# Optimization experiments

Measured on AMD Instinct MI355X. Metric: run time of the kernel, lower is better.

## Reference

```python
import jax, jax.numpy as jnp
import numpy as np
import math

T, B, D, H, FF = 2048, 2, 1024, 16, 4096
HD = D // H
STD = 0.02


def _gelu(x):
    # SongNet gelu: tanh approximation
    return 0.5 * x * (1.0 + jnp.tanh(math.sqrt(2.0 / math.pi) * (x + 0.044715 * x ** 3)))


def _layer_norm(x, g, b, eps=1e-5):
    mu = jnp.mean(x, axis=-1, keepdims=True)
    var = jnp.mean((x - mu) ** 2, axis=-1, keepdims=True)
    return (x - mu) * jax.lax.rsqrt(var + eps) * g + b


def setup_inputs() -> dict:
    key = jax.random.key(0)
    ks = jax.random.split(key, 6)
    return {
        "x": jax.random.normal(ks[0], (T, B, D), jnp.float32),
        "attn_mask": jnp.triu(jnp.ones((T, T), bool), k=1),  # True = masked (causal)
        "in_proj_w": jax.random.normal(ks[1], (3 * D, D), jnp.float32) * STD,
        "in_proj_b": jnp.zeros((3 * D,), jnp.float32),
        "out_w": jax.random.normal(ks[2], (D, D), jnp.float32) * STD,
        "out_b": jnp.zeros((D,), jnp.float32),
        "fc1_w": jax.random.normal(ks[3], (FF, D), jnp.float32) * STD,
        "fc1_b": jnp.zeros((FF,), jnp.float32),
        "fc2_w": jax.random.normal(ks[4], (D, FF), jnp.float32) * STD,
        "fc2_b": jnp.zeros((D,), jnp.float32),
        "ln1_g": jnp.ones((D,), jnp.float32),
        "ln1_b": jnp.zeros((D,), jnp.float32),
        "ln2_g": jnp.ones((D,), jnp.float32),
        "ln2_b": jnp.zeros((D,), jnp.float32),
    }


def reference(x, attn_mask, in_proj_w, in_proj_b, out_w, out_b,
              fc1_w, fc1_b, fc2_w, fc2_b, ln1_g, ln1_b, ln2_g, ln2_b):
    t, b, d = x.shape
    scaling = HD ** -0.5
    # fused in-proj (qkv_same path): [T,B,3D]
    qkv = x @ in_proj_w.T + in_proj_b
    q, k, v = jnp.split(qkv, 3, axis=-1)
    q = q * scaling

    def to_heads(z):  # [T,B,D] -> [B*H, T, HD]
        return z.reshape(t, b * H, HD).transpose(1, 0, 2)

    q, k, v = to_heads(q), to_heads(k), to_heads(v)
    # [B*H, T, T] attention scores (full matrix, as in original bmm)
    scores = jnp.einsum('nth,nsh->nts', q, k)
    scores = jnp.where(attn_mask[None, :, :], -jnp.inf, scores)
    w = jax.nn.softmax(scores, axis=-1)
    attn = jnp.einsum('nts,nsh->nth', w, v)          # [B*H, T, HD]
    attn = attn.transpose(1, 0, 2).reshape(t, b, d)  # [T,B,D]
    attn = attn @ out_w.T + out_b

    h = _layer_norm(x + attn, ln1_g, ln1_b)
    ff = _gelu(h @ fc1_w.T + fc1_b) @ fc2_w.T + fc2_b
    out = _layer_norm(h + ff, ln2_g, ln2_b)
    return out
```

## Files before the change

### kernel.cpp

```cpp
#include <hip/hip_runtime.h>
#include <hip/hip_bf16.h>
#include <math.h>


typedef __bf16 bf16x8_t __attribute__((ext_vector_type(8)));
typedef __bf16 bf16x4_t __attribute__((ext_vector_type(4)));
typedef float  f32x4_t  __attribute__((ext_vector_type(4)));

#define T_  2048
#define B_  2
#define D_  1024
#define H_  16
#define HD_ 64
#define FF_ 4096
#define M_  (T_ * B_)

#define LOG2E 1.4426950408889634f
#define SCL   (0.125f * LOG2E)

__device__ __forceinline__ float gelu_f(float v) {
    const float y = 0.79788456080286535588f * (v + 0.044715f * v * v * v);
    const float t = __builtin_amdgcn_exp2f(-2.8853900817779268f * y);
    return v * __builtin_amdgcn_rcpf(1.0f + t);
}

__device__ __forceinline__ void gld_lds16(const void* g, void* l) {
    __builtin_amdgcn_global_load_lds((const __attribute__((address_space(1))) void*)g,
                                     (__attribute__((address_space(3))) void*)l, 16, 0, 0);
}

template<int MODE, int OWNM>
__global__ __launch_bounds__(256, 4)
void gemm_bt(const __bf16* __restrict__ A, const __bf16* __restrict__ W,
             const float* __restrict__ bias, float* __restrict__ Cf0,
             float* __restrict__ Cf1, __bf16* __restrict__ Cb, int M, int N, int K)
{
    __shared__ __align__(16) __bf16 As[128 * 32];
    __shared__ __align__(16) __bf16 Bs[128 * 32];
    const int tid  = threadIdx.x;
    const int lane = tid & 63;
    const int wave = tid >> 6;
    const int quad = lane >> 4;
    const int l15  = lane & 15;

    const int gx = gridDim.x, gy = gridDim.y;
    int flat = ((int)blockIdx.z * gy + (int)blockIdx.y) * gx + (int)blockIdx.x;
    int bx, by, z;
    if (OWNM) {
        const int P = gy >> 3;
        const int x = flat & 7; int s = flat >> 3;
        by = x * P + (s % P); s /= P;
        bx = s % gx; z = s / gx;
    } else {
        const int P = gx >> 3;
        const int x = flat & 7; int s = flat >> 3;
        bx = x * P + (s % P); s /= P;
        by = s % gy; z = s / gy;
    }
    const int m0 = by * 128;
    const int n0 = bx * 128;
    const int wm = (wave >> 1) * 64;
    const int wn = (wave & 1) * 64;
    const int Kloc = K / (int)gridDim.z;
    const int kbeg = z * Kloc;

    const int srow = wave * 32 + (lane >> 2);
    const int scol = (((lane & 3) ^ ((lane >> 3) & 3))) * 8;
    const __bf16* gA = A + (size_t)(m0 + srow) * K + scol;
    const __bf16* gB = W + (size_t)(n0 + srow) * K + scol;
    const size_t rowK16 = (size_t)16 * K;
    __bf16* ldsA0 = As + wave * 1024;
    __bf16* ldsA1 = As + wave * 1024 + 512;
    __bf16* ldsB0 = Bs + wave * 1024;
    __bf16* ldsB1 = Bs + wave * 1024 + 512;

    const int asw = (quad ^ ((l15 >> 1) & 3)) * 8;

    f32x4_t acc[4][4] = {};

    for (int kb = kbeg; kb < kbeg + Kloc; kb += 32) {
        gld_lds16(gA + kb,          ldsA0);
        gld_lds16(gA + kb + rowK16, ldsA1);
        gld_lds16(gB + kb,          ldsB0);
        gld_lds16(gB + kb + rowK16, ldsB1);
        __syncthreads();
        bf16x8_t af[4], bfr[4];
        #pragma unroll
        for (int i = 0; i < 4; ++i) af[i]  = *(const bf16x8_t*)&As[(wm + i * 16 + l15) * 32 + asw];
        #pragma unroll
        for (int i = 0; i < 4; ++i) bfr[i] = *(const bf16x8_t*)&Bs[(wn + i * 16 + l15) * 32 + asw];
        #pragma unroll
        for (int mi = 0; mi < 4; ++mi)
            #pragma unroll
            for (int ni = 0; ni < 4; ++ni)
                acc[mi][ni] = __builtin_amdgcn_mfma_f32_16x16x32_bf16(af[mi], bfr[ni], acc[mi][ni], 0, 0, 0);
        __syncthreads();
    }

    float* __restrict__ Cf = (z == 0) ? Cf0 : Cf1;
    #pragma unroll
    for (int mi = 0; mi < 4; ++mi) {
        const int row = m0 + wm + mi * 16 + quad * 4;
        #pragma unroll
        for (int ni = 0; ni < 4; ++ni) {
            const int col = n0 + wn + ni * 16 + l15;
            const float bv = (z == 0) ? bias[col] : 0.f;
            #pragma unroll
            for (int r = 0; r < 4; ++r) {
                float v = acc[mi][ni][r] + bv;
                if (MODE == 2) v = gelu_f(v);
                if (MODE == 0) Cf[(size_t)(row + r) * N + col] = v;
                else           Cb[(size_t)(row + r) * N + col] = (__bf16)v;
            }
        }
    }
}

__global__ __launch_bounds__(256)
void vtrans_kernel(const __bf16* __restrict__ qkv, __bf16* __restrict__ vt)
{
    __shared__ __bf16 S[64][72];
    const int tt = blockIdx.x, bh = blockIdx.y;
    const int b = bh >> 4, h = bh & 15;
    const int tid = threadIdx.x;
    const int tl = tid >> 2, ch = (tid & 3) * 16;
    const __bf16* src = qkv + ((size_t)(tt * 64 + tl) * B_ + b) * (3 * D_) + 2 * D_ + h * HD_ + ch;
    *(bf16x8_t*)&S[tl][ch]     = *(const bf16x8_t*)src;
    *(bf16x8_t*)&S[tl][ch + 8] = *(const bf16x8_t*)(src + 8);
    __syncthreads();
    #pragma unroll
    for (int p = 0; p < 2; ++p) {
        const int hd = p * 32 + (tid >> 3);
        const int tc = (tid & 7) * 8;
        bf16x8_t v;
        #pragma unroll
        for (int j = 0; j < 8; ++j) v[j] = S[tc + j][hd];
        *(bf16x8_t*)(vt + ((size_t)bh * 64 + hd) * T_ + tt * 64 + tc) = v;
    }
}

__global__ __launch_bounds__(256)
void attn_kernel(const __bf16* __restrict__ qkv, const __bf16* __restrict__ vt,
                 __bf16* __restrict__ attnout)
{
    const int bh = blockIdx.y;
    const int b  = bh >> 4;
    const int h  = bh & 15;
    const int tid  = threadIdx.x;
    const int lane = tid & 63;
    const int wave = tid >> 6;
    const int quad = lane >> 4;
    const int l15  = lane & 15;

    __shared__ __align__(16) __bf16 Ks[64 * 64];
    __shared__ __align__(16) __bf16 Vs[64 * 64];
    __shared__ __align__(16) __bf16 Ps[4][16 * 64];

    const int kr = lane >> 3;
    const int kc = (lane & 7) ^ kr;
    const size_t krow = (size_t)B_ * 3 * D_;
    const __bf16* gK0 = qkv + ((size_t)(wave * 16 + kr) * B_ + b) * (3 * D_) + D_ + h * HD_ + kc * 8;
    const __bf16* gV0 = vt + ((size_t)bh * 64 + wave * 16 + kr) * T_ + kc * 8;
    __bf16* ldsK0 = &Ks[wave * 16 * 64];
    __bf16* ldsK1 = &Ks[wave * 16 * 64 + 8 * 64];
    __bf16* ldsV0 = &Vs[wave * 16 * 64];
    __bf16* ldsV1 = &Vs[wave * 16 * 64 + 8 * 64];
    const int ksw = l15 & 7;

    const bf16x8_t ONES = {(__bf16)1.f, (__bf16)1.f, (__bf16)1.f, (__bf16)1.f,
                           (__bf16)1.f, (__bf16)1.f, (__bf16)1.f, (__bf16)1.f};

    for (int ph = 0; ph < 2; ++ph) {
        const int qt = (ph == 0) ? (31 - (int)blockIdx.x) : (int)blockIdx.x;
        const int q0 = qt * 64;
        const int tq = q0 + wave * 16 + l15;
        const __bf16* qbase = qkv + ((size_t)tq * B_ + b) * (3 * D_) + h * HD_;
        bf16x8_t aq0 = *(const bf16x8_t*)(qbase + quad * 8);
        bf16x8_t aq1 = *(const bf16x8_t*)(qbase + 32 + quad * 8);

        f32x4_t o[4] = {};
        f32x4_t lacc = {};

        for (int kt = 0; kt <= qt; ++kt) {
            const int s0 = kt * 64;
            __syncthreads();
            gld_lds16(gK0 + (size_t)s0 * krow,       ldsK0);
            gld_lds16(gK0 + (size_t)(s0 + 8) * krow, ldsK1);
            gld_lds16(gV0 + s0,                      ldsV0);
            gld_lds16(gV0 + (size_t)8 * T_ + s0,     ldsV1);
            __syncthreads();

            f32x4_t sc[4] = {};
            #pragma unroll
            for (int ni = 0; ni < 4; ++ni) {
                const int rb = (ni * 16 + l15) * 64;
                bf16x8_t kf0 = *(const bf16x8_t*)&Ks[rb + ((quad ^ ksw) & 7) * 8];
                bf16x8_t kf1 = *(const bf16x8_t*)&Ks[rb + (((quad + 4) ^ ksw) & 7) * 8];
                sc[ni] = __builtin_amdgcn_mfma_f32_16x16x32_bf16(aq0, kf0, sc[ni], 0, 0, 0);
                sc[ni] = __builtin_amdgcn_mfma_f32_16x16x32_bf16(aq1, kf1, sc[ni], 0, 0, 0);
            }

            const bool diag = (kt == qt);
            #pragma unroll
            for (int ni = 0; ni < 4; ++ni) {
                #pragma unroll
                for (int r = 0; r < 4; ++r) {
                    float pv = __builtin_amdgcn_exp2f(sc[ni][r] * SCL);
                    if (diag) {
                        const int tr_ = wave * 16 + quad * 4 + r;
                        pv = ((ni * 16 + l15) <= tr_) ? pv : 0.f;
                    }
                    const int row = quad * 4 + r;
                    const int ch = ((ni * 2 + (l15 >> 3)) + (row >> 1)) & 7;
                    Ps[wave][row * 64 + ch * 8 + (l15 & 7)] = (__bf16)pv;
                }
            }
            bf16x8_t ap0 = *(const bf16x8_t*)&Ps[wave][l15 * 64 + ((quad + (l15 >> 1)) & 7) * 8];
            bf16x8_t ap1 = *(const bf16x8_t*)&Ps[wave][l15 * 64 + ((quad + 4 + (l15 >> 1)) & 7) * 8];

            lacc = __builtin_amdgcn_mfma_f32_16x16x32_bf16(ap0, ONES, lacc, 0, 0, 0);
            lacc = __builtin_amdgcn_mfma_f32_16x16x32_bf16(ap1, ONES, lacc, 0, 0, 0);

            #pragma unroll
            for (int ni = 0; ni < 4; ++ni) {
                const int rbv = (ni * 16 + l15) * 64;
                bf16x8_t bv0 = *(const bf16x8_t*)&Vs[rbv + ((quad ^ ksw) & 7) * 8];
                bf16x8_t bv1 = *(const bf16x8_t*)&Vs[rbv + (((quad + 4) ^ ksw) & 7) * 8];
                o[ni] = __builtin_amdgcn_mfma_f32_16x16x32_bf16(ap0, bv0, o[ni], 0, 0, 0);
                o[ni] = __builtin_amdgcn_mfma_f32_16x16x32_bf16(ap1, bv1, o[ni], 0, 0, 0);
            }
        }

        float linv[4];
        #pragma unroll
        for (int r = 0; r < 4; ++r) linv[r] = __builtin_amdgcn_rcpf(lacc[r]);
        #pragma unroll
        for (int ni = 0; ni < 4; ++ni) {
            #pragma unroll
            for (int r = 0; r < 4; ++r) {
                const int tr = q0 + wave * 16 + quad * 4 + r;
                attnout[((size_t)tr * B_ + b) * D_ + h * HD_ + ni * 16 + l15] =
                    (__bf16)(o[ni][r] * linv[r]);
            }
        }
    }
}

__global__ __launch_bounds__(256)
void ln3_kernel(const float* __restrict__ A, const float* __restrict__ R0,
                const float* __restrict__ R1,
                const float* __restrict__ g, const float* __restrict__ bb,
                float* __restrict__ outf, __bf16* __restrict__ outb)
{
    const int row = blockIdx.x;
    const int tid = threadIdx.x;
    const float4 va = ((const float4*)(A  + (size_t)row * D_))[tid];
    const float4 v0 = ((const float4*)(R0 + (size_t)row * D_))[tid];
    const float4 v1 = ((const float4*)(R1 + (size_t)row * D_))[tid];
    const float z0 = va.x + v0.x + v1.x, z1 = va.y + v0.y + v1.y;
    const float z2 = va.z + v0.z + v1.z, z3 = va.w + v0.w + v1.w;
    float s  = z0 + z1 + z2 + z3;
    float ss = z0 * z0 + z1 * z1 + z2 * z2 + z3 * z3;
    #pragma unroll
    for (int off = 1; off < 64; off <<= 1) {
        s  += __shfl_xor(s, off, 64);
        ss += __shfl_xor(ss, off, 64);
    }
    __shared__ float rs[4], rss[4];
    const int wv = tid >> 6, lane = tid & 63;
    if (lane == 0) { rs[wv] = s; rss[wv] = ss; }
    __syncthreads();
    s  = rs[0] + rs[1] + rs[2] + rs[3];
    ss = rss[0] + rss[1] + rss[2] + rss[3];
    const float mu   = s * (1.f / D_);
    const float var  = ss * (1.f / D_) - mu * mu;
    const float rstd = rsqrtf(var + 1e-5f);
    const float4 vg = ((const float4*)g)[tid];
    const float4 vb = ((const float4*)bb)[tid];
    const float o0 = (z0 - mu) * rstd * vg.x + vb.x;
    const float o1 = (z1 - mu) * rstd * vg.y + vb.y;
    const float o2 = (z2 - mu) * rstd * vg.z + vb.z;
    const float o3 = (z3 - mu) * rstd * vg.w + vb.w;
    ((float4*)(outf + (size_t)row * D_))[tid] = make_float4(o0, o1, o2, o3);
    if (outb) {
        bf16x4_t ob;
        ob[0] = (__bf16)o0; ob[1] = (__bf16)o1; ob[2] = (__bf16)o2; ob[3] = (__bf16)o3;
        ((bf16x4_t*)(outb + (size_t)row * D_))[tid] = ob;
    }
}

__global__ __launch_bounds__(256)
void cvt_kernel(const float* __restrict__ in, __bf16* __restrict__ out, int n4)
{
    const int i = blockIdx.x * 256 + threadIdx.x;
    if (i >= n4) return;
    const float4 v = ((const float4*)in)[i];
    bf16x4_t ob;
    ob[0] = (__bf16)v.x; ob[1] = (__bf16)v.y; ob[2] = (__bf16)v.z; ob[3] = (__bf16)v.w;
    ((bf16x4_t*)out)[i] = ob;
}

extern "C" void kernel_launch(void* const* d_in, const int* in_sizes, int n_in,
                              void* d_out, int out_size, void* d_ws, size_t ws_size,
                              hipStream_t stream)
{
    (void)in_sizes; (void)n_in; (void)out_size; (void)ws_size;
    const float* x         = (const float*)d_in[0];
    const float* in_proj_w = (const float*)d_in[2];
    const float* in_proj_b = (const float*)d_in[3];
    const float* out_w     = (const float*)d_in[4];
    const float* out_b     = (const float*)d_in[5];
    const float* fc1_w     = (const float*)d_in[6];
    const float* fc1_b     = (const float*)d_in[7];
    const float* fc2_w     = (const float*)d_in[8];
    const float* fc2_b     = (const float*)d_in[9];
    const float* ln1_g     = (const float*)d_in[10];
    const float* ln1_b     = (const float*)d_in[11];
    const float* ln2_g     = (const float*)d_in[12];
    const float* ln2_b     = (const float*)d_in[13];

    char* p = (char*)d_ws;
    __bf16* regA = (__bf16*)p; p += (size_t)M_ * D_ * 2;
    __bf16* hb   = (__bf16*)p; p += (size_t)M_ * D_ * 2;
    float*  yf2  = (float*)regA;
    __bf16* wreg = (__bf16*)p; p += (size_t)FF_ * D_ * 2;
    __bf16* qkvb = (__bf16*)p;
    __bf16* g1b  = qkvb;       p += (size_t)M_ * FF_ * 2;
    float*  yf   = (float*)p;  p += (size_t)M_ * D_ * 4;
    float*  hf   = (float*)p;  p += (size_t)M_ * D_ * 4;
    __bf16* vt   = (__bf16*)yf;

    const dim3 blk(256);

    cvt_kernel<<<dim3((M_ * D_ / 4) / 256), blk, 0, stream>>>(x, regA, M_ * D_ / 4);
    cvt_kernel<<<dim3((3 * D_ * D_ / 4) / 256), blk, 0, stream>>>(in_proj_w, wreg, 3 * D_ * D_ / 4);
    gemm_bt<1, 1><<<dim3(3 * D_ / 128, M_ / 128, 1), blk, 0, stream>>>(
        regA, wreg, in_proj_b, nullptr, nullptr, qkvb, M_, 3 * D_, D_);

    vtrans_kernel<<<dim3(T_ / 64, B_ * H_), blk, 0, stream>>>(qkvb, vt);
    attn_kernel<<<dim3(T_ / 128, B_ * H_), blk, 0, stream>>>(qkvb, vt, regA);

    cvt_kernel<<<dim3((D_ * D_ / 4) / 256), blk, 0, stream>>>(out_w, wreg, D_ * D_ / 4);
    gemm_bt<0, 1><<<dim3(D_ / 128, M_ / 128, 2), blk, 0, stream>>>(
        regA, wreg, out_b, yf, hf, nullptr, M_, D_, D_);

    ln3_kernel<<<dim3(M_), blk, 0, stream>>>(x, yf, hf, ln1_g, ln1_b, hf, hb);

    cvt_kernel<<<dim3((FF_ * D_ / 4) / 256), blk, 0, stream>>>(fc1_w, wreg, FF_ * D_ / 4);
    gemm_bt<2, 0><<<dim3(FF_ / 128, M_ / 128, 1), blk, 0, stream>>>(
        hb, wreg, fc1_b, nullptr, nullptr, g1b, M_, FF_, D_);

    cvt_kernel<<<dim3((D_ * FF_ / 4) / 256), blk, 0, stream>>>(fc2_w, wreg, D_ * FF_ / 4);
    gemm_bt<0, 1><<<dim3(D_ / 128, M_ / 128, 2), blk, 0, stream>>>(
        g1b, wreg, fc2_b, yf, yf2, nullptr, M_, D_, FF_);

    ln3_kernel<<<dim3(M_), blk, 0, stream>>>(hf, yf, yf2, ln2_g, ln2_b, (float*)d_out, nullptr);
}
```

Measured before the change: 365.2 us.

## Deepen GEMM K-tile, share K/V tiles across paired query tiles, merge weight casts

```diff
diff --git a/kernel.cpp b/kernel.cpp
--- a/kernel.cpp
+++ b/kernel.cpp
@@ -35,8 +35,8 @@
              const float* __restrict__ bias, float* __restrict__ Cf0,
              float* __restrict__ Cf1, __bf16* __restrict__ Cb, int M, int N, int K)
 {
-    __shared__ __align__(16) __bf16 As[128 * 32];
-    __shared__ __align__(16) __bf16 Bs[128 * 32];
+    __shared__ __align__(16) __bf16 As[128 * 64];
+    __shared__ __align__(16) __bf16 Bs[128 * 64];
     const int tid  = threadIdx.x;
     const int lane = tid & 63;
     const int wave = tid >> 6;
@@ -64,36 +64,39 @@
     const int Kloc = K / (int)gridDim.z;
     const int kbeg = z * Kloc;
 
-    const int srow = wave * 32 + (lane >> 2);
-    const int scol = (((lane & 3) ^ ((lane >> 3) & 3))) * 8;
-    const __bf16* gA = A + (size_t)(m0 + srow) * K + scol;
-    const __bf16* gB = W + (size_t)(n0 + srow) * K + scol;
-    const size_t rowK16 = (size_t)16 * K;
-    __bf16* ldsA0 = As + wave * 1024;
-    __bf16* ldsA1 = As + wave * 1024 + 512;
-    __bf16* ldsB0 = Bs + wave * 1024;
-    __bf16* ldsB1 = Bs + wave * 1024 + 512;
-
-    const int asw = (quad ^ ((l15 >> 1) & 3)) * 8;
+    const int srow8 = lane >> 3;
+    const int scol  = ((lane & 7) ^ srow8) * 8;
+    const __bf16* gA = A + (size_t)(m0 + wave * 32 + srow8) * K + scol;
+    const __bf16* gB = W + (size_t)(n0 + wave * 32 + srow8) * K + scol;
+    const size_t row8K = (size_t)8 * K;
+    __bf16* ldsA = As + wave * 2048;
+    __bf16* ldsB = Bs + wave * 2048;
+
+    const int fsw = l15 & 7;
 
     f32x4_t acc[4][4] = {};
 
-    for (int kb = kbeg; kb < kbeg + Kloc; kb += 32) {
-        gld_lds16(gA + kb,          ldsA0);
-        gld_lds16(gA + kb + rowK16, ldsA1);
-        gld_lds16(gB + kb,          ldsB0);
-        gld_lds16(gB + kb + rowK16, ldsB1);
+    for (int kb = kbeg; kb < kbeg + Kloc; kb += 64) {
+        #pragma unroll
+        for (int j = 0; j < 4; ++j) {
+            gld_lds16(gA + kb + j * row8K, ldsA + j * 512);
+            gld_lds16(gB + kb + j * row8K, ldsB + j * 512);
+        }
         __syncthreads();
-        bf16x8_t af[4], bfr[4];
-        #pragma unroll
-        for (int i = 0; i < 4; ++i) af[i]  = *(const bf16x8_t*)&As[(wm + i * 16 + l15) * 32 + asw];
-        #pragma unroll
-        for (int i = 0; i < 4; ++i) bfr[i] = *(const bf16x8_t*)&Bs[(wn + i * 16 + l15) * 32 + asw];
-        #pragma unroll
-        for (int mi = 0; mi < 4; ++mi)
-            #pragma unroll
-            for (int ni = 0; ni < 4; ++ni)
-                acc[mi][ni] = __builtin_amdgcn_mfma_f32_16x16x32_bf16(af[mi], bfr[ni], acc[mi][ni], 0, 0, 0);
+        #pragma unroll
+        for (int half = 0; half < 2; ++half) {
+            const int co = ((quad + half * 4) ^ fsw) * 8;
+            bf16x8_t af[4], bfr[4];
+            #pragma unroll
+            for (int i = 0; i < 4; ++i) af[i]  = *(const bf16x8_t*)&As[(wm + i * 16 + l15) * 64 + co];
+            #pragma unroll
+            for (int i = 0; i < 4; ++i) bfr[i] = *(const bf16x8_t*)&Bs[(wn + i * 16 + l15) * 64 + co];
+            #pragma unroll
+            for (int mi = 0; mi < 4; ++mi)
+                #pragma unroll
+                for (int ni = 0; ni < 4; ++ni)
+                    acc[mi][ni] = __builtin_amdgcn_mfma_f32_16x16x32_bf16(af[mi], bfr[ni], acc[mi][ni], 0, 0, 0);
+        }
         __syncthreads();
     }
 
@@ -136,6 +139,57 @@
         #pragma unroll
         for (int j = 0; j < 8; ++j) v[j] = S[tc + j][hd];
         *(bf16x8_t*)(vt + ((size_t)bh * 64 + hd) * T_ + tt * 64 + tc) = v;
+    }
+}
+
+struct QState {
+    bf16x8_t aq0, aq1;
+    f32x4_t  o[4];
+    f32x4_t  lacc;
+};
+
+__device__ __forceinline__ void attn_tile_step(
+    QState& st, const __bf16* __restrict__ Ks, const __bf16* __restrict__ Vs,
+    __bf16* __restrict__ Psw, bool diag, int wave, int quad, int l15, int ksw)
+{
+    const bf16x8_t ONES = {(__bf16)1.f, (__bf16)1.f, (__bf16)1.f, (__bf16)1.f,
+                           (__bf16)1.f, (__bf16)1.f, (__bf16)1.f, (__bf16)1.f};
+    f32x4_t sc[4] = {};
+    #pragma unroll
+    for (int ni = 0; ni < 4; ++ni) {
+        const int rb = (ni * 16 + l15) * 64;
+        bf16x8_t kf0 = *(const bf16x8_t*)&Ks[rb + ((quad ^ ksw) & 7) * 8];
+        bf16x8_t kf1 = *(const bf16x8_t*)&Ks[rb + (((quad + 4) ^ ksw) & 7) * 8];
+        sc[ni] = __builtin_amdgcn_mfma_f32_16x16x32_bf16(st.aq0, kf0, sc[ni], 0, 0, 0);
+        sc[ni] = __builtin_amdgcn_mfma_f32_16x16x32_bf16(st.aq1, kf1, sc[ni], 0, 0, 0);
+    }
+    #pragma unroll
+    for (int ni = 0; ni < 4; ++ni) {
+        #pragma unroll
+        for (int r = 0; r < 4; ++r) {
+            float pv = __builtin_amdgcn_exp2f(sc[ni][r] * SCL);
+            if (diag) {
+                const int tr_ = wave * 16 + quad * 4 + r;
+                pv = ((ni * 16 + l15) <= tr_) ? pv : 0.f;
+            }
+            const int row = quad * 4 + r;
+            const int ch = ((ni * 2 + (l15 >> 3)) + (row >> 1)) & 7;
+            Psw[row * 64 + ch * 8 + (l15 & 7)] = (__bf16)pv;
+        }
+    }
+    bf16x8_t ap0 = *(const bf16x8_t*)&Psw[l15 * 64 + ((quad + (l15 >> 1)) & 7) * 8];
+    bf16x8_t ap1 = *(const bf16x8_t*)&Psw[l15 * 64 + ((quad + 4 + (l15 >> 1)) & 7) * 8];
+
+    st.lacc = __builtin_amdgcn_mfma_f32_16x16x32_bf16(ap0, ONES, st.lacc, 0, 0, 0);
+    st.lacc = __builtin_amdgcn_mfma_f32_16x16x32_bf16(ap1, ONES, st.lacc, 0, 0, 0);
+
+    #pragma unroll
+    for (int ni = 0; ni < 4; ++ni) {
+        const int rbv = (ni * 16 + l15) * 64;
+        bf16x8_t bv0 = *(const bf16x8_t*)&Vs[rbv + ((quad ^ ksw) & 7) * 8];
+        bf16x8_t bv1 = *(const bf16x8_t*)&Vs[rbv + (((quad + 4) ^ ksw) & 7) * 8];
+        st.o[ni] = __builtin_amdgcn_mfma_f32_16x16x32_bf16(ap0, bv0, st.o[ni], 0, 0, 0);
+        st.o[ni] = __builtin_amdgcn_mfma_f32_16x16x32_bf16(ap1, bv1, st.o[ni], 0, 0, 0);
     }
 }
 
@@ -166,81 +220,51 @@
     __bf16* ldsV0 = &Vs[wave * 16 * 64];
     __bf16* ldsV1 = &Vs[wave * 16 * 64 + 8 * 64];
     const int ksw = l15 & 7;
-
-    const bf16x8_t ONES = {(__bf16)1.f, (__bf16)1.f, (__bf16)1.f, (__bf16)1.f,
-                           (__bf16)1.f, (__bf16)1.f, (__bf16)1.f, (__bf16)1.f};
-
-    for (int ph = 0; ph < 2; ++ph) {
-        const int qt = (ph == 0) ? (31 - (int)blockIdx.x) : (int)blockIdx.x;
-        const int q0 = qt * 64;
-        const int tq = q0 + wave * 16 + l15;
-        const __bf16* qbase = qkv + ((size_t)tq * B_ + b) * (3 * D_) + h * HD_;
-        bf16x8_t aq0 = *(const bf16x8_t*)(qbase + quad * 8);
-        bf16x8_t aq1 = *(const bf16x8_t*)(qbase + 32 + quad * 8);
-
-        f32x4_t o[4] = {};
-        f32x4_t lacc = {};
-
-        for (int kt = 0; kt <= qt; ++kt) {
-            const int s0 = kt * 64;
-            __syncthreads();
-            gld_lds16(gK0 + (size_t)s0 * krow,       ldsK0);
-            gld_lds16(gK0 + (size_t)(s0 + 8) * krow, ldsK1);
-            gld_lds16(gV0 + s0,                      ldsV0);
-            gld_lds16(gV0 + (size_t)8 * T_ + s0,     ldsV1);
-            __syncthreads();
-
-            f32x4_t sc[4] = {};
-            #pragma unroll
-            for (int ni = 0; ni < 4; ++ni) {
-                const int rb = (ni * 16 + l15) * 64;
-                bf16x8_t kf0 = *(const bf16x8_t*)&Ks[rb + ((quad ^ ksw) & 7) * 8];
-                bf16x8_t kf1 = *(const bf16x8_t*)&Ks[rb + (((quad + 4) ^ ksw) & 7) * 8];
-                sc[ni] = __builtin_amdgcn_mfma_f32_16x16x32_bf16(aq0, kf0, sc[ni], 0, 0, 0);
-                sc[ni] = __builtin_amdgcn_mfma_f32_16x16x32_bf16(aq1, kf1, sc[ni], 0, 0, 0);
-            }
-
-            const bool diag = (kt == qt);
-            #pragma unroll
-            for (int ni = 0; ni < 4; ++ni) {
-                #pragma unroll
-                for (int r = 0; r < 4; ++r) {
-                    float pv = __builtin_amdgcn_exp2f(sc[ni][r] * SCL);
-                    if (diag) {
-                        const int tr_ = wave * 16 + quad * 4 + r;
-                        pv = ((ni * 16 + l15) <= tr_) ? pv : 0.f;
-                    }
-                    const int row = quad * 4 + r;
-                    const int ch = ((ni * 2 + (l15 >> 3)) + (row >> 1)) & 7;
-                    Ps[wave][row * 64 + ch * 8 + (l15 & 7)] = (__bf16)pv;
-                }
-            }
-            bf16x8_t ap0 = *(const bf16x8_t*)&Ps[wave][l15 * 64 + ((quad + (l15 >> 1)) & 7) * 8];
-            bf16x8_t ap1 = *(const bf16x8_t*)&Ps[wave][l15 * 64 + ((quad + 4 + (l15 >> 1)) & 7) * 8];
-
-            lacc = __builtin_amdgcn_mfma_f32_16x16x32_bf16(ap0, ONES, lacc, 0, 0, 0);
-            lacc = __builtin_amdgcn_mfma_f32_16x16x32_bf16(ap1, ONES, lacc, 0, 0, 0);
-
-            #pragma unroll
-            for (int ni = 0; ni < 4; ++ni) {
-                const int rbv = (ni * 16 + l15) * 64;
-                bf16x8_t bv0 = *(const bf16x8_t*)&Vs[rbv + ((quad ^ ksw) & 7) * 8];
-                bf16x8_t bv1 = *(const bf16x8_t*)&Vs[rbv + (((quad + 4) ^ ksw) & 7) * 8];
-                o[ni] = __builtin_amdgcn_mfma_f32_16x16x32_bf16(ap0, bv0, o[ni], 0, 0, 0);
-                o[ni] = __builtin_amdgcn_mfma_f32_16x16x32_bf16(ap1, bv1, o[ni], 0, 0, 0);
-            }
-        }
-
+    __bf16* Psw = &Ps[wave][0];
+
+    const int qtA = 31 - (int)blockIdx.x;
+    const int qtB = (int)blockIdx.x;
+
+    QState stA = {}, stB = {};
+    {
+        const int tqA = qtA * 64 + wave * 16 + l15;
+        const __bf16* qbA = qkv + ((size_t)tqA * B_ + b) * (3 * D_) + h * HD_;
+        stA.aq0 = *(const bf16x8_t*)(qbA + quad * 8);
+        stA.aq1 = *(const bf16x8_t*)(qbA + 32 + quad * 8);
+        const int tqB = qtB * 64 + wave * 16 + l15;
+        const __bf16* qbB = qkv + ((size_t)tqB * B_ + b) * (3 * D_) + h * HD_;
+        stB.aq0 = *(const bf16x8_t*)(qbB + quad * 8);
+        stB.aq1 = *(const bf16x8_t*)(qbB + 32 + quad * 8);
+    }
+
+    for (int kt = 0; kt <= qtA; ++kt) {
+        const int s0 = kt * 64;
+        __syncthreads();
+        gld_lds16(gK0 + (size_t)s0 * krow,       ldsK0);
+        gld_lds16(gK0 + (size_t)(s0 + 8) * krow, ldsK1);
+        gld_lds16(gV0 + s0,                      ldsV0);
+        gld_lds16(gV0 + (size_t)8 * T_ + s0,     ldsV1);
+        __syncthreads();
+
+        attn_tile_step(stA, Ks, Vs, Psw, kt == qtA, wave, quad, l15, ksw);
+        if (kt <= qtB)
+            attn_tile_step(stB, Ks, Vs, Psw, kt == qtB, wave, quad, l15, ksw);
+    }
+
+    #pragma unroll
+    for (int t = 0; t < 2; ++t) {
+        const QState& st = t ? stB : stA;
+        const int q0 = (t ? qtB : qtA) * 64;
         float linv[4];
         #pragma unroll
-        for (int r = 0; r < 4; ++r) linv[r] = __builtin_amdgcn_rcpf(lacc[r]);
+        for (int r = 0; r < 4; ++r) linv[r] = __builtin_amdgcn_rcpf(st.lacc[r]);
         #pragma unroll
         for (int ni = 0; ni < 4; ++ni) {
             #pragma unroll
             for (int r = 0; r < 4; ++r) {
                 const int tr = q0 + wave * 16 + quad * 4 + r;
                 attnout[((size_t)tr * B_ + b) * D_ + h * HD_ + ni * 16 + l15] =
-                    (__bf16)(o[ni][r] * linv[r]);
+                    (__bf16)(st.o[ni][r] * linv[r]);
             }
         }
     }
@@ -290,14 +314,20 @@
 }
 
 __global__ __launch_bounds__(256)
-void cvt_kernel(const float* __restrict__ in, __bf16* __restrict__ out, int n4)
-{
-    const int i = blockIdx.x * 256 + threadIdx.x;
-    if (i >= n4) return;
-    const float4 v = ((const float4*)in)[i];
+void cvt3_kernel(const float* __restrict__ s0, __bf16* __restrict__ d0, int n0,
+                 const float* __restrict__ s1, __bf16* __restrict__ d1, int n1,
+                 const float* __restrict__ s2, __bf16* __restrict__ d2, int n2)
+{
+    int i = blockIdx.x * 256 + threadIdx.x;
+    const float* s; __bf16* d;
+    if (i < n0) { s = s0; d = d0; }
+    else if ((i -= n0) < n1) { s = s1; d = d1; }
+    else if ((i -= n1) < n2) { s = s2; d = d2; }
+    else return;
+    const float4 v = ((const float4*)s)[i];
     bf16x4_t ob;
     ob[0] = (__bf16)v.x; ob[1] = (__bf16)v.y; ob[2] = (__bf16)v.z; ob[3] = (__bf16)v.w;
-    ((bf16x4_t*)out)[i] = ob;
+    ((bf16x4_t*)d)[i] = ob;
 }
 
 extern "C" void kernel_launch(void* const* d_in, const int* in_sizes, int n_in,
@@ -329,28 +359,34 @@
     float*  yf   = (float*)p;  p += (size_t)M_ * D_ * 4;
     float*  hf   = (float*)p;  p += (size_t)M_ * D_ * 4;
     __bf16* vt   = (__bf16*)yf;
+    __bf16* outwb = wreg + (size_t)3 * D_ * D_;
 
     const dim3 blk(256);
 
-    cvt_kernel<<<dim3((M_ * D_ / 4) / 256), blk, 0, stream>>>(x, regA, M_ * D_ / 4);
-    cvt_kernel<<<dim3((3 * D_ * D_ / 4) / 256), blk, 0, stream>>>(in_proj_w, wreg, 3 * D_ * D_ / 4);
+    {
+        const int nx = M_ * D_ / 4, ni = 3 * D_ * D_ / 4, no = D_ * D_ / 4;
+        cvt3_kernel<<<dim3((nx + ni + no) / 256), blk, 0, stream>>>(
+            x, regA, nx, in_proj_w, wreg, ni, out_w, outwb, no);
+    }
+
     gemm_bt<1, 1><<<dim3(3 * D_ / 128, M_ / 128, 1), blk, 0, stream>>>(
         regA, wreg, in_proj_b, nullptr, nullptr, qkvb, M_, 3 * D_, D_);
 
     vtrans_kernel<<<dim3(T_ / 64, B_ * H_), blk, 0, stream>>>(qkvb, vt);
     attn_kernel<<<dim3(T_ / 128, B_ * H_), blk, 0, stream>>>(qkvb, vt, regA);
 
-    cvt_kernel<<<dim3((D_ * D_ / 4) / 256), blk, 0, stream>>>(out_w, wreg, D_ * D_ / 4);
     gemm_bt<0, 1><<<dim3(D_ / 128, M_ / 128, 2), blk, 0, stream>>>(
-        regA, wreg, out_b, yf, hf, nullptr, M_, D_, D_);
+        regA, outwb, out_b, yf, hf, nullptr, M_, D_, D_);
 
     ln3_kernel<<<dim3(M_), blk, 0, stream>>>(x, yf, hf, ln1_g, ln1_b, hf, hb);
 
-    cvt_kernel<<<dim3((FF_ * D_ / 4) / 256), blk, 0, stream>>>(fc1_w, wreg, FF_ * D_ / 4);
+    cvt3_kernel<<<dim3((FF_ * D_ / 4) / 256), blk, 0, stream>>>(
+        fc1_w, wreg, FF_ * D_ / 4, nullptr, nullptr, 0, nullptr, nullptr, 0);
     gemm_bt<2, 0><<<dim3(FF_ / 128, M_ / 128, 1), blk, 0, stream>>>(
         hb, wreg, fc1_b, nullptr, nullptr, g1b, M_, FF_, D_);
 
-    cvt_kernel<<<dim3((D_ * FF_ / 4) / 256), blk, 0, stream>>>(fc2_w, wreg, D_ * FF_ / 4);
+    cvt3_kernel<<<dim3((D_ * FF_ / 4) / 256), blk, 0, stream>>>(
+        fc2_w, wreg, D_ * FF_ / 4, nullptr, nullptr, 0, nullptr, nullptr, 0);
     gemm_bt<0, 1><<<dim3(D_ / 128, M_ / 128, 2), blk, 0, stream>>>(
         g1b, wreg, fc2_b, yf, yf2, nullptr, M_, D_, FF_);
 
```

New measurement: 351.2 us. -3.8%, faster.
